# Optimization experiments

Hardware: AMD Instinct MI355X
Metric: run time of the kernel (lower is better)

## Reference

```python
import jax, jax.numpy as jnp
import numpy as np

B, CIN, X, Y = 4, 3, 128, 128
D, L, DEPTH, OUT = 64, 8, 4, 1
GRID_RANGE = 1.0
LN_EPS = 1e-5
YR = Y // 2 + 1


def _build_phi_f():
    # 1D Hilbert-matrix eigenbases along each axis, outer product, then rfft2.
    def top_eigvecs(n):
        i = np.arange(n)
        Z = 1.0 / (i[:, None] + i[None, :] + 1.0)  # Hilbert matrix, float64
        w, V = np.linalg.eigh(Z)
        idx = np.argsort(-w)[:L]
        return V.T[idx]  # (L, n)

    Vx = top_eigvecs(X)
    Vy = top_eigvecs(Y)
    phi = Vx[:, :, None] * Vy[:, None, :]  # (L, X, Y) separable eigenfunctions
    Phi_f = np.fft.rfft2(phi, s=(X, Y))  # (L, X, YR)
    return jnp.asarray(Phi_f, dtype=jnp.complex64)


def setup_inputs() -> dict:
    key = jax.random.key(0)
    ks = jax.random.split(key, 16)
    u = lambda k, shape, bound: jax.random.uniform(k, shape, jnp.float32, -bound, bound)
    inv = 1.0 / np.sqrt(D)
    inp = {
        "x": jax.random.normal(ks[0], (B, CIN, X, Y), jnp.float32),
        "Phi_f": _build_phi_f(),  # constant buffer
        "lift_w": u(ks[1], (D, CIN + 2), 1.0 / np.sqrt(CIN + 2)),
        "lift_b": u(ks[2], (D,), 1.0 / np.sqrt(CIN + 2)),
        "Theta": u(ks[3], (DEPTH, L, D, D), 1.0 / D),  # kaiming_uniform(a=sqrt(5)) ~ U(-1/d, 1/d)
        "glu_val_w": u(ks[4], (DEPTH, D, D), inv),
        "glu_val_b": u(ks[5], (DEPTH, D), inv),
        "glu_gate_w": u(ks[6], (DEPTH, D, D), inv),
        "glu_gate_b": u(ks[7], (DEPTH, D), inv),
        "ln_g": jnp.ones((DEPTH, D), jnp.float32),
        "ln_b": jnp.zeros((DEPTH, D), jnp.float32),
        "head_w": u(ks[8], (OUT, D), inv),
        "head_b": u(ks[9], (OUT,), inv),
    }
    return inp


def _stu_layer(h, Phi_f, Theta, vw, vb, gw, gb, g, b):
    # LayerNorm over channel dim (torch LayerNorm on channels-last view)
    ht = jnp.transpose(h, (0, 2, 3, 1))  # (B, X, Y, D)
    mu = jnp.mean(ht, axis=-1, keepdims=True)
    var = jnp.var(ht, axis=-1, keepdims=True)
    zt = (ht - mu) * jax.lax.rsqrt(var + LN_EPS) * g + b
    z = jnp.transpose(zt, (0, 3, 1, 2))  # (B, D, X, Y)

    Xf = jnp.fft.rfftn(z, axes=(-2, -1))  # (B, D, X, YR) complex
    Uf = Xf[:, :, None, :, :] * jnp.conj(Phi_f)[None, None]  # (B, D, L, X, YR)
    U = jnp.fft.irfftn(Uf, s=(X, Y), axes=(-2, -1))  # (B, D, L, X, Y)
    # einsum('bdlxy,lhd->bhlxy') followed by sum over l, fused:
    S = jnp.einsum("bdlxy,lhd->bhxy", U, Theta)

    V = jnp.einsum("bhxy,oh->boxy", S, vw) + vb[None, :, None, None]
    G = jax.nn.sigmoid(jnp.einsum("bhxy,oh->boxy", S, gw) + gb[None, :, None, None])
    return h + V * G


def reference(x, Phi_f, lift_w, lift_b, Theta, glu_val_w, glu_val_b,
              glu_gate_w, glu_gate_b, ln_g, ln_b, head_w, head_b):
    bsz = x.shape[0]
    # add_2d_grid: append yy, xx coordinate channels
    ys = jnp.linspace(0.0, GRID_RANGE, X, dtype=x.dtype)
    xs = jnp.linspace(0.0, GRID_RANGE, Y, dtype=x.dtype)
    yy, xx = jnp.meshgrid(ys, xs, indexing="ij")
    yy = jnp.broadcast_to(yy[None, None], (bsz, 1, X, Y))
    xx = jnp.broadcast_to(xx[None, None], (bsz, 1, X, Y))
    h = jnp.concatenate([x, yy, xx], axis=1)  # (B, CIN+2, X, Y)

    # LocalLift2D with kernel_size=1 -> pointwise conv
    h = jnp.einsum("bcxy,dc->bdxy", h, lift_w) + lift_b[None, :, None, None]

    for i in range(DEPTH):
        h = _stu_layer(h, Phi_f, Theta[i], glu_val_w[i], glu_val_b[i],
                       glu_gate_w[i], glu_gate_b[i], ln_g[i], ln_b[i])

    y = jnp.einsum("bdxy,od->boxy", h, head_w) + head_b[None, :, None, None]
    return y
```

## Files before the change

### kernel.cpp

```cpp
#include <hip/hip_runtime.h>
#include <math.h>
#include <string.h>


#define NXY 16384

#define OFF_V       16
#define OFF_MC      1040
#define OFF_THETAA  132112
#define OFF_AG      263184
#define OFF_Z       295952
#define OFF_S       2393104
#define OFF_H       4490256
#define OFF_P       8684560
#define WS_NEED_F   25461776ULL

typedef short short8 __attribute__((ext_vector_type(8)));
typedef float float4m __attribute__((ext_vector_type(4)));

__device__ __forceinline__ unsigned short bf_rn(float f) {
    unsigned u = __float_as_uint(f);
    u += 0x7fffu + ((u >> 16) & 1u);
    return (unsigned short)(u >> 16);
}
__device__ __forceinline__ float bf_tof(unsigned short s) {
    return __uint_as_float(((unsigned)s) << 16);
}

__global__ void poison_out(float* out) { out[0] = 1e9f; }


static float vhost[1024];
static float* d_v_dev = nullptr;

static void host_hilbert_topk(float* outv) {
    static double Vs[8][128];
    static double W[8][128];
    double recip[256];
    for (int i = 0; i < 256; i++) recip[i] = 1.0 / (double)(i + 1);
    for (int j = 0; j < 8; j++)
        for (int i = 0; i < 128; i++) Vs[j][i] = recip[i + j];
    for (int outer = 0; outer < 25; outer++) {
        for (int half = 0; half < 2; half++) {
            for (int j = 0; j < 8; j++)
                for (int i = 0; i < 128; i++) {
                    double s = 0.0;
                    for (int k = 0; k < 128; k++) s += Vs[j][k] * recip[i + k];
                    W[j][i] = s;
                }
            memcpy(Vs, W, sizeof(Vs));
        }
        for (int j = 0; j < 8; j++) {
            for (int p = 0; p < j; p++) {
                double d = 0.0;
                for (int i = 0; i < 128; i++) d += Vs[j][i] * Vs[p][i];
                for (int i = 0; i < 128; i++) Vs[j][i] -= d * Vs[p][i];
            }
            double nn = 0.0;
            for (int i = 0; i < 128; i++) nn += Vs[j][i] * Vs[j][i];
            double inv = 1.0 / sqrt(nn);
            for (int i = 0; i < 128; i++) Vs[j][i] *= inv;
        }
    }
    for (int j = 0; j < 8; j++)
        for (int i = 0; i < 128; i++) outv[j * 128 + i] = (float)Vs[j][i];
}

namespace {
struct VInit {
    VInit() {
        host_hilbert_topk(vhost);
        float* p = nullptr;
        if (hipMalloc((void**)&p, sizeof(vhost)) == hipSuccess && p != nullptr) {
            if (hipMemcpy(p, vhost, sizeof(vhost), hipMemcpyHostToDevice) == hipSuccess) {
                d_v_dev = p;
            } else {
                (void)hipFree(p);
                d_v_dev = nullptr;
            }
        }
    }
};
VInit vinit_once;
}

__global__ void build_mct(const float* __restrict__ v, unsigned short* __restrict__ McT) {
    int l = blockIdx.y;
    int idx = blockIdx.x * 256 + threadIdx.x;
    int r = idx >> 7, k = idx & 127;
    McT[l * 16384 + idx] = bf_rn(v[l * 128 + ((k - r) & 127)]);
}


__global__ void build_thetaAHL(const float* __restrict__ Theta, unsigned short* __restrict__ ThA) {
    int i = blockIdx.x * 256 + threadIdx.x;
    int k = i & 127; int r = i >> 7;
    int m = r & 127; r >>= 7;
    int tile = r & 3; int dep = r >> 2;
    int l2 = m >> 6, hch = m & 63, d = k & 63;
    float f = Theta[(((dep * 8 + tile * 2 + l2) * 64) + hch) * 64 + d];
    unsigned short hb = bf_rn(f);
    ThA[i] = (k < 64) ? hb : bf_rn(f - bf_tof(hb));
}

__global__ void build_AG(const float* __restrict__ vw, const float* __restrict__ gw,
                         float* __restrict__ AG) {
    int i = blockIdx.x * 256 + threadIdx.x;
    int m = i & 127; int r = i >> 7; int h = r & 63; int dep = r >> 6;
    int o = m >> 1;
    const float* W = (m & 1) ? gw : vw;
    AG[i] = W[(dep * 64 + o) * 64 + h];
}


__global__ void lift_ln(const float* __restrict__ x, const float* __restrict__ lw,
                        const float* __restrict__ lb, const float* __restrict__ g0,
                        const float* __restrict__ b0, float* __restrict__ h,
                        unsigned short* __restrict__ zT) {
    __shared__ float w[320];
    __shared__ float bsm[64];
    __shared__ float gs[64], bs[64];
    int tid = threadIdx.x;
    for (int i = tid; i < 320; i += 256) w[i] = lw[i];
    if (tid < 64) { bsm[tid] = lb[tid]; gs[tid] = g0[tid]; bs[tid] = b0[tid]; }
    __syncthreads();
    int b = blockIdx.y;
    int xy = blockIdx.x * 256 + tid;
    int xi = xy >> 7, yi = xy & 127;
    float c0 = x[(size_t)(b * 3 + 0) * NXY + xy];
    float c1 = x[(size_t)(b * 3 + 1) * NXY + xy];
    float c2 = x[(size_t)(b * 3 + 2) * NXY + xy];
    float yyv = xi * (1.0f / 127.0f), xxv = yi * (1.0f / 127.0f);
    float vv[64];
    float sum = 0.f;
#pragma unroll
    for (int d = 0; d < 64; d++) {
        float acc = bsm[d] + w[d * 5] * c0 + w[d * 5 + 1] * c1 + w[d * 5 + 2] * c2
                  + w[d * 5 + 3] * yyv + w[d * 5 + 4] * xxv;
        vv[d] = acc;
        sum += acc;
        h[(size_t)(b * 64 + d) * NXY + xy] = acc;
    }
    float mu = sum * (1.0f / 64.0f);
    float vs = 0.f;
#pragma unroll
    for (int d = 0; d < 64; d++) { float t = vv[d] - mu; vs += t * t; }
    float inv = rsqrtf(vs * (1.0f / 64.0f) + 1e-5f);
    unsigned short t16[64];
#pragma unroll
    for (int d = 0; d < 64; d++) t16[d] = bf_rn((vv[d] - mu) * inv * gs[d] + bs[d]);
    unsigned short* zp = zT + ((size_t)b * NXY + xy) * 64;
#pragma unroll
    for (int i = 0; i < 8; i++) {
        uint4 pk;
        pk.x = (unsigned)t16[8 * i + 0] | ((unsigned)t16[8 * i + 1] << 16);
        pk.y = (unsigned)t16[8 * i + 2] | ((unsigned)t16[8 * i + 3] << 16);
        pk.z = (unsigned)t16[8 * i + 4] | ((unsigned)t16[8 * i + 5] << 16);
        pk.w = (unsigned)t16[8 * i + 6] | ((unsigned)t16[8 * i + 7] << 16);
        *(uint4*)(zp + 8 * i) = pk;
    }
}

__device__ __forceinline__ int sw_idx(int row, int k) {
    return row * 128 + ((((k >> 3) ^ (row & 7)) << 3) | (k & 7));
}
__device__ __forceinline__ int sw64(int row, int k) {
    return row * 64 + (((((k >> 3) ^ (row & 7)) & 7) << 3) | (k & 7));
}


__launch_bounds__(256)
__global__ void k1_mfma(const unsigned short* __restrict__ zT,
                        const unsigned short* __restrict__ ThA,
                        unsigned short* __restrict__ P) {
    __shared__ unsigned short st[16384];
    const int lhtile = blockIdx.x, x = blockIdx.y, b = blockIdx.z;
    const int tid = threadIdx.x;
    const int wid = tid >> 6, lane = tid & 63;
    const int ln15 = lane & 15, q = lane >> 4;
    const int ko = q * 8;
    const unsigned short* Ab = ThA + lhtile * 16384;
    const unsigned short* Bb = zT + ((size_t)b * NXY + x * 128) * 64;

    float4m acc[2][8];
#pragma unroll
    for (int mt = 0; mt < 2; mt++)
#pragma unroll
        for (int nt = 0; nt < 8; nt++) acc[mt][nt] = (float4m){0.f, 0.f, 0.f, 0.f};

#pragma unroll
    for (int k0 = 0; k0 < 128; k0 += 32) {
        short8 a[2];
#pragma unroll
        for (int mt = 0; mt < 2; mt++)
            a[mt] = *(const short8*)(Ab + (wid * 32 + mt * 16 + ln15) * 128 + k0 + ko);
        int d0 = (k0 & 63) + ko;
#pragma unroll
        for (int nt = 0; nt < 8; nt++) {
            int n = nt * 16 + ln15;
            short8 bf = *(const short8*)(Bb + n * 64 + d0);
#pragma unroll
            for (int mt = 0; mt < 2; mt++)
                acc[mt][nt] = __builtin_amdgcn_mfma_f32_16x16x32_bf16(a[mt], bf, acc[mt][nt], 0, 0, 0);
        }
    }
#pragma unroll
    for (int mt = 0; mt < 2; mt++)
#pragma unroll
        for (int nt = 0; nt < 8; nt++) {
            int y = nt * 16 + ln15;
            int r0 = wid * 32 + mt * 16 + q * 4;
            float av[4] = {acc[mt][nt].x, acc[mt][nt].y, acc[mt][nt].z, acc[mt][nt].w};
#pragma unroll
            for (int r = 0; r < 4; r++) st[sw_idx(r0 + r, y)] = bf_rn(av[r]);
        }
    __syncthreads();
    unsigned short* Pb = P + (size_t)(b * 512 + lhtile * 128) * NXY + x * 128;
#pragma unroll
    for (int i = 0; i < 8; i++) {
        int idx = i * 256 + tid;
        int m = idx >> 4, c = idx & 15;
        *(uint4*)(Pb + (size_t)m * NXY + c * 8) = *(const uint4*)&st[sw_idx(m, c * 8)];
    }
}


__launch_bounds__(256)
__global__ void corrsum_ys(const unsigned short* __restrict__ P,
                           const unsigned short* __restrict__ McT,
                           unsigned short* __restrict__ S) {
    __shared__ unsigned short Tt[8192];
    const int hh = blockIdx.x, yh = blockIdx.y, b = blockIdx.z;
    const int tid = threadIdx.x;
    const int wid = tid >> 6, lane = tid & 63;
    const int ln15 = lane & 15, q = lane >> 4;
    const int ko = q * 8;
    const int mrow0 = wid * 32 + ln15;
    const int yb = yh * 64;

    float4m accS[2][4];
#pragma unroll
    for (int mt = 0; mt < 2; mt++)
#pragma unroll
        for (int nt = 0; nt < 4; nt++) accS[mt][nt] = (float4m){0.f, 0.f, 0.f, 0.f};

    short8 apre[2][4][2];

    {
        const unsigned short* pl = P + ((size_t)(b * 8 + 0) * 64 + hh) * NXY;
#pragma unroll
        for (int k4 = 0; k4 < 4; k4++)
#pragma unroll
            for (int mt = 0; mt < 2; mt++)
                apre[0][k4][mt] = *(const short8*)(pl + (mrow0 + mt * 16) * 128 + k4 * 32 + ko);
    }

#pragma unroll
    for (int l = 0; l < 8; l++) {
        const unsigned short* Mc = McT + l * 16384;
        const int cb = l & 1, nb = cb ^ 1;

        float4m acc1[2][4];
#pragma unroll
        for (int mt = 0; mt < 2; mt++)
#pragma unroll
            for (int nt = 0; nt < 4; nt++) acc1[mt][nt] = (float4m){0.f, 0.f, 0.f, 0.f};
#pragma unroll
        for (int k4 = 0; k4 < 4; k4++) {
            int k0 = k4 * 32;
#pragma unroll
            for (int nt = 0; nt < 4; nt++) {
                int n = yb + nt * 16 + ln15;
                short8 bf = *(const short8*)(Mc + n * 128 + k0 + ko);
#pragma unroll
                for (int mt = 0; mt < 2; mt++)
                    acc1[mt][nt] = __builtin_amdgcn_mfma_f32_16x16x32_bf16(apre[cb][k4][mt], bf, acc1[mt][nt], 0, 0, 0);
            }
        }
#pragma unroll
        for (int mt = 0; mt < 2; mt++)
#pragma unroll
            for (int nt = 0; nt < 4; nt++) {
                int yo = nt * 16 + ln15;
                int x0 = wid * 32 + mt * 16 + q * 4;
                float av[4] = {acc1[mt][nt].x, acc1[mt][nt].y, acc1[mt][nt].z, acc1[mt][nt].w};
                unsigned short hs[4];
#pragma unroll
                for (int r = 0; r < 4; r++) hs[r] = bf_rn(av[r]);
                uint2 pk;
                pk.x = (unsigned)hs[0] | ((unsigned)hs[1] << 16);
                pk.y = (unsigned)hs[2] | ((unsigned)hs[3] << 16);
                *(uint2*)&Tt[sw_idx(yo, x0)] = pk;
            }
        __syncthreads();

        if (l < 7) {
            const unsigned short* pln = P + ((size_t)(b * 8 + l + 1) * 64 + hh) * NXY;
#pragma unroll
            for (int k4 = 0; k4 < 4; k4++)
#pragma unroll
                for (int mt = 0; mt < 2; mt++)
                    apre[nb][k4][mt] = *(const short8*)(pln + (mrow0 + mt * 16) * 128 + k4 * 32 + ko);
        }

#pragma unroll
        for (int k4 = 0; k4 < 4; k4++) {
            int k0 = k4 * 32;
            short8 a2[2];
#pragma unroll
            for (int mt = 0; mt < 2; mt++)
                a2[mt] = *(const short8*)(Mc + (mrow0 + mt * 16) * 128 + k0 + ko);
#pragma unroll
            for (int nt = 0; nt < 4; nt++) {
                int n = nt * 16 + ln15;
                short8 bf = *(const short8*)&Tt[sw_idx(n, k0 + ko)];
#pragma unroll
                for (int mt = 0; mt < 2; mt++)
                    accS[mt][nt] = __builtin_amdgcn_mfma_f32_16x16x32_bf16(a2[mt], bf, accS[mt][nt], 0, 0, 0);
            }
        }
        __syncthreads();
    }

#pragma unroll
    for (int mt = 0; mt < 2; mt++)
#pragma unroll
        for (int nt = 0; nt < 4; nt++) {
            int yl = nt * 16 + ln15;
            int x0 = wid * 32 + mt * 16 + q * 4;
            float av[4] = {accS[mt][nt].x, accS[mt][nt].y, accS[mt][nt].z, accS[mt][nt].w};
#pragma unroll
            for (int r = 0; r < 4; r++) Tt[sw64(x0 + r, yl)] = bf_rn(av[r]);
        }
    __syncthreads();
    unsigned short* Sb = S + ((size_t)(b * 64) + hh) * NXY + yb;
#pragma unroll
    for (int i = 0; i < 4; i++) {
        int idx = i * 256 + tid;
        int xr = idx >> 3, c = idx & 7;
        *(uint4*)(Sb + xr * 128 + c * 8) = *(const uint4*)&Tt[sw64(xr, c * 8)];
    }
}


template <int KTOT, long long BS1, long long PSTR, int NPART>
__launch_bounds__(256)
__global__ void glu_ln(const float* __restrict__ A0,
                       const unsigned short* __restrict__ B0, long long bsx, long long bsz,
                       float* __restrict__ C0, long long csx, long long csz, long long csm,
                       const float* __restrict__ e_vb, const float* __restrict__ e_gb,
                       const float* __restrict__ lngn, const float* __restrict__ lnbn,
                       unsigned short* __restrict__ zT,
                       const float* __restrict__ hw, const float* __restrict__ hbp,
                       float* __restrict__ outp) {
    constexpr int KS = 16;
    __shared__ float As[KS][132];
    __shared__ float Bs[KS][132];
    __shared__ float hn[64][129];
    const int tid = threadIdx.x;
    const int tm = tid >> 4, tn = tid & 15;
    const int m0 = tm * 8, n0 = tn * 8;
    const float* Ab = A0;
    const unsigned short* Bb = B0 + (long long)blockIdx.x * bsx + (long long)blockIdx.z * bsz;
    float* Cb = C0 + (long long)blockIdx.x * csx + (long long)blockIdx.z * csz;

    float acc[8][8];
#pragma unroll
    for (int i = 0; i < 8; i++)
#pragma unroll
        for (int j = 0; j < 8; j++) acc[i][j] = 0.f;

    for (int k0 = 0; k0 < KTOT; k0 += KS) {
#pragma unroll
        for (int i = 0; i < 2; i++) {
            int idx = tid + i * 256;
            int k = idx >> 5, f4 = (idx & 31) * 4;
            float4 v = *(const float4*)(Ab + (long long)(k0 + k) * 128 + f4);
            *(float4*)&As[k][f4] = v;
        }
#pragma unroll
        for (int i = 0; i < 2; i++) {
            int idx = tid + i * 256;
            int k = idx >> 5, f4 = (idx & 31) * 4;
            const unsigned short* bp = Bb + (long long)(k0 + k) * BS1 + f4;
            float vx = 0.f, vy = 0.f, vz = 0.f, vw = 0.f;
#pragma unroll
            for (int p = 0; p < NPART; p++) {
                uint2 t = *(const uint2*)(bp + (long long)p * PSTR);
                vx += bf_tof((unsigned short)(t.x & 0xffff));
                vy += bf_tof((unsigned short)(t.x >> 16));
                vz += bf_tof((unsigned short)(t.y & 0xffff));
                vw += bf_tof((unsigned short)(t.y >> 16));
            }
            Bs[k][f4] = vx; Bs[k][f4 + 1] = vy; Bs[k][f4 + 2] = vz; Bs[k][f4 + 3] = vw;
        }
        __syncthreads();
#pragma unroll
        for (int kk = 0; kk < KS; kk++) {
            float4 a0 = *(const float4*)&As[kk][m0];
            float4 a1 = *(const float4*)&As[kk][m0 + 4];
            float4 b0 = *(const float4*)&Bs[kk][n0];
            float4 b1 = *(const float4*)&Bs[kk][n0 + 4];
            float av[8] = {a0.x, a0.y, a0.z, a0.w, a1.x, a1.y, a1.z, a1.w};
            float bv[8] = {b0.x, b0.y, b0.z, b0.w, b1.x, b1.y, b1.z, b1.w};
#pragma unroll
            for (int i = 0; i < 8; i++)
#pragma unroll
                for (int j = 0; j < 8; j++) acc[i][j] += av[i] * bv[j];
        }
        __syncthreads();
    }

#pragma unroll
    for (int i = 0; i < 4; i++) {
        int o = (m0 >> 1) + i;
        float vbv = e_vb[o], gbv = e_gb[o];
        float* hp = Cb + (long long)o * csm + n0;
        float4 h0 = *(float4*)hp;
        float4 h1 = *(float4*)(hp + 4);
        float hv[8] = {h0.x, h0.y, h0.z, h0.w, h1.x, h1.y, h1.z, h1.w};
#pragma unroll
        for (int j = 0; j < 8; j++) {
            float V = acc[2 * i][j] + vbv;
            float G = acc[2 * i + 1][j] + gbv;
            float s = 1.0f / (1.0f + expf(-G));
            hv[j] += V * s;
            hn[o][n0 + j] = hv[j];
        }
        if (outp == nullptr) {
            float4 o0 = {hv[0], hv[1], hv[2], hv[3]};
            float4 o1 = {hv[4], hv[5], hv[6], hv[7]};
            *(float4*)hp = o0;
            *(float4*)(hp + 4) = o1;
        }
    }

    if (lngn != nullptr) {
        __syncthreads();
        if (tid < 128) {
            int xy = tid;
            float sum = 0.f;
#pragma unroll
            for (int d = 0; d < 64; d++) sum += hn[d][xy];
            float mu = sum * (1.0f / 64.0f);
            float vs = 0.f;
#pragma unroll
            for (int d = 0; d < 64; d++) { float t = hn[d][xy] - mu; vs += t * t; }
            float inv = rsqrtf(vs * (1.0f / 64.0f) + 1e-5f);
            unsigned short t16[64];
#pragma unroll
            for (int d = 0; d < 64; d++)
                t16[d] = bf_rn((hn[d][xy] - mu) * inv * lngn[d] + lnbn[d]);
            unsigned short* zp = zT + ((size_t)blockIdx.z * NXY + blockIdx.x * 128 + xy) * 64;
#pragma unroll
            for (int i = 0; i < 8; i++) {
                uint4 pk;
                pk.x = (unsigned)t16[8 * i + 0] | ((unsigned)t16[8 * i + 1] << 16);
                pk.y = (unsigned)t16[8 * i + 2] | ((unsigned)t16[8 * i + 3] << 16);
                pk.z = (unsigned)t16[8 * i + 4] | ((unsigned)t16[8 * i + 5] << 16);
                pk.w = (unsigned)t16[8 * i + 6] | ((unsigned)t16[8 * i + 7] << 16);
                *(uint4*)(zp + 8 * i) = pk;
            }
        }
    } else if (outp != nullptr) {
        __syncthreads();
        if (tid < 128) {
            int xy = tid;
            float acch = hbp[0];
#pragma unroll
            for (int d = 0; d < 64; d++) acch += hn[d][xy] * hw[d];
            outp[(size_t)blockIdx.z * NXY + blockIdx.x * 128 + xy] = acch;
        }
    }
}


extern "C" void kernel_launch(void* const* d_in, const int* in_sizes, int n_in,
                              void* d_out, int out_size, void* d_ws, size_t ws_size,
                              hipStream_t stream) {
    const float* x      = (const float*)d_in[0];
    const float* lift_w = (const float*)d_in[2];
    const float* lift_b = (const float*)d_in[3];
    const float* Theta  = (const float*)d_in[4];
    const float* vw     = (const float*)d_in[5];
    const float* vb     = (const float*)d_in[6];
    const float* gw     = (const float*)d_in[7];
    const float* gb     = (const float*)d_in[8];
    const float* ln_g   = (const float*)d_in[9];
    const float* ln_b   = (const float*)d_in[10];
    const float* head_w = (const float*)d_in[11];
    const float* head_b = (const float*)d_in[12];
    float* out = (float*)d_out;
    float* ws = (float*)d_ws;
    (void)in_sizes; (void)n_in; (void)out_size;

    unsigned short* McT = (unsigned short*)(ws + OFF_MC);
    unsigned short* ThA = (unsigned short*)(ws + OFF_THETAA);
    float* AG     = ws + OFF_AG;
    unsigned short* zT = (unsigned short*)(ws + OFF_Z);
    unsigned short* S  = (unsigned short*)(ws + OFF_S);
    float* h      = ws + OFF_H;
    unsigned short* P = (unsigned short*)(ws + OFF_P);

    const float* vdev = d_v_dev;
    if (vdev == nullptr) {
        float* v = ws + OFF_V;
        hipMemcpyAsync(v, vhost, sizeof(vhost), hipMemcpyHostToDevice, stream);
        vdev = v;
    }

    build_mct<<<dim3(64, 8), 256, 0, stream>>>(vdev, McT);
    build_thetaAHL<<<1024, 256, 0, stream>>>(Theta, ThA);
    build_AG<<<128, 256, 0, stream>>>(vw, gw, AG);

    lift_ln<<<dim3(64, 4), 256, 0, stream>>>(x, lift_w, lift_b, ln_g, ln_b, h, zT);

    for (int dep = 0; dep < 4; dep++) {
        k1_mfma<<<dim3(4, 128, 4), 256, 0, stream>>>(zT, ThA + dep * 65536, P);

        corrsum_ys<<<dim3(64, 2, 4), 256, 0, stream>>>(P, McT, S);

        const float* lngn = (dep < 3) ? (ln_g + (dep + 1) * 64) : nullptr;
        const float* lnbn = (dep < 3) ? (ln_b + (dep + 1) * 64) : nullptr;
        float* outp = (dep == 3) ? out : nullptr;
        glu_ln<64, 16384LL, 0LL, 1><<<dim3(128, 1, 4), 256, 0, stream>>>(
            AG + dep * 8192,
            S, 128, 1048576,
            h, 128, 1048576, 16384,
            vb + dep * 64, gb + dep * 64,
            lngn, lnbn, zT,
            head_w, head_b, outp);
    }

    if (ws_size < WS_NEED_F * 4ULL) {
        poison_out<<<1, 1, 0, stream>>>(out);
    }
}
```

Baseline: 553.8 us.

## Split correlation second GEMM over K per wave to remove per-iteration barriers

The second-stage GEMM in the correlation kernel is restructured so each wave contracts only over its own 32 x-rows (its K slice) into a full 128x64 partial accumulator. This removes the two __syncthreads per l-iteration, since each wave only reads the Tt region it wrote itself. A shared-memory reduction across the four waves is added at the end. The trade-off is a much larger accumulator footprint per wave (32 float4 tiles), which raises register pressure, plus 32KB of extra LDS and a serial 3-step merge. The software prefetch of the next P plane is also dropped.

```diff
diff --git a/kernel.cpp b/kernel.cpp
--- a/kernel.cpp
+++ b/kernel.cpp
@@ -226,39 +226,36 @@
 
 
 __launch_bounds__(256)
-__global__ void corrsum_ys(const unsigned short* __restrict__ P,
-                           const unsigned short* __restrict__ McT,
-                           unsigned short* __restrict__ S) {
+__global__ void corr_nb(const unsigned short* __restrict__ P,
+                        const unsigned short* __restrict__ McT,
+                        unsigned short* __restrict__ S) {
     __shared__ unsigned short Tt[8192];
+    __shared__ float Mrg[8192];
     const int hh = blockIdx.x, yh = blockIdx.y, b = blockIdx.z;
     const int tid = threadIdx.x;
     const int wid = tid >> 6, lane = tid & 63;
     const int ln15 = lane & 15, q = lane >> 4;
     const int ko = q * 8;
-    const int mrow0 = wid * 32 + ln15;
+    const int xq0 = wid * 32;
     const int yb = yh * 64;
 
-    float4m accS[2][4];
-#pragma unroll
-    for (int mt = 0; mt < 2; mt++)
-#pragma unroll
-        for (int nt = 0; nt < 4; nt++) accS[mt][nt] = (float4m){0.f, 0.f, 0.f, 0.f};
-
-    short8 apre[2][4][2];
-
-    {
-        const unsigned short* pl = P + ((size_t)(b * 8 + 0) * 64 + hh) * NXY;
-#pragma unroll
-        for (int k4 = 0; k4 < 4; k4++)
-#pragma unroll
-            for (int mt = 0; mt < 2; mt++)
-                apre[0][k4][mt] = *(const short8*)(pl + (mrow0 + mt * 16) * 128 + k4 * 32 + ko);
-    }
+    float4m acc[8][4];
+#pragma unroll
+    for (int mtu = 0; mtu < 8; mtu++)
+#pragma unroll
+        for (int nt = 0; nt < 4; nt++) acc[mtu][nt] = (float4m){0.f, 0.f, 0.f, 0.f};
 
 #pragma unroll
     for (int l = 0; l < 8; l++) {
         const unsigned short* Mc = McT + l * 16384;
-        const int cb = l & 1, nb = cb ^ 1;
+        const unsigned short* pl = P + ((size_t)(b * 8 + l) * 64 + hh) * NXY;
+
+        short8 ap[4][2];
+#pragma unroll
+        for (int k4 = 0; k4 < 4; k4++)
+#pragma unroll
+            for (int mt = 0; mt < 2; mt++)
+                ap[k4][mt] = *(const short8*)(pl + (xq0 + mt * 16 + ln15) * 128 + k4 * 32 + ko);
 
         float4m acc1[2][4];
 #pragma unroll
@@ -274,7 +271,7 @@
                 short8 bf = *(const short8*)(Mc + n * 128 + k0 + ko);
 #pragma unroll
                 for (int mt = 0; mt < 2; mt++)
-                    acc1[mt][nt] = __builtin_amdgcn_mfma_f32_16x16x32_bf16(apre[cb][k4][mt], bf, acc1[mt][nt], 0, 0, 0);
+                    acc1[mt][nt] = __builtin_amdgcn_mfma_f32_16x16x32_bf16(ap[k4][mt], bf, acc1[mt][nt], 0, 0, 0);
             }
         }
 #pragma unroll
@@ -282,7 +279,7 @@
 #pragma unroll
             for (int nt = 0; nt < 4; nt++) {
                 int yo = nt * 16 + ln15;
-                int x0 = wid * 32 + mt * 16 + q * 4;
+                int x0 = xq0 + mt * 16 + q * 4;
                 float av[4] = {acc1[mt][nt].x, acc1[mt][nt].y, acc1[mt][nt].z, acc1[mt][nt].w};
                 unsigned short hs[4];
 #pragma unroll
@@ -292,46 +289,63 @@
                 pk.y = (unsigned)hs[2] | ((unsigned)hs[3] << 16);
                 *(uint2*)&Tt[sw_idx(yo, x0)] = pk;
             }
+
+        short8 a2[8];
+#pragma unroll
+        for (int mtu = 0; mtu < 8; mtu++)
+            a2[mtu] = *(const short8*)(Mc + (mtu * 16 + ln15) * 128 + xq0 + ko);
+#pragma unroll
+        for (int nt = 0; nt < 4; nt++) {
+            short8 bf = *(const short8*)&Tt[sw_idx(nt * 16 + ln15, xq0 + ko)];
+#pragma unroll
+            for (int mtu = 0; mtu < 8; mtu++)
+                acc[mtu][nt] = __builtin_amdgcn_mfma_f32_16x16x32_bf16(a2[mtu], bf, acc[mtu][nt], 0, 0, 0);
+        }
+    }
+
+    __syncthreads();
+#pragma unroll
+    for (int src = 1; src < 4; src++) {
+        if (wid == src) {
+#pragma unroll
+            for (int mtu = 0; mtu < 8; mtu++)
+#pragma unroll
+                for (int nt = 0; nt < 4; nt++) {
+                    int v0 = (mtu * 4 + nt) * 4;
+                    Mrg[(v0 + 0) * 64 + lane] = acc[mtu][nt].x;
+                    Mrg[(v0 + 1) * 64 + lane] = acc[mtu][nt].y;
+                    Mrg[(v0 + 2) * 64 + lane] = acc[mtu][nt].z;
+                    Mrg[(v0 + 3) * 64 + lane] = acc[mtu][nt].w;
+                }
+        }
         __syncthreads();
-
-        if (l < 7) {
-            const unsigned short* pln = P + ((size_t)(b * 8 + l + 1) * 64 + hh) * NXY;
-#pragma unroll
-            for (int k4 = 0; k4 < 4; k4++)
-#pragma unroll
-                for (int mt = 0; mt < 2; mt++)
-                    apre[nb][k4][mt] = *(const short8*)(pln + (mrow0 + mt * 16) * 128 + k4 * 32 + ko);
-        }
-
-#pragma unroll
-        for (int k4 = 0; k4 < 4; k4++) {
-            int k0 = k4 * 32;
-            short8 a2[2];
-#pragma unroll
-            for (int mt = 0; mt < 2; mt++)
-                a2[mt] = *(const short8*)(Mc + (mrow0 + mt * 16) * 128 + k0 + ko);
+        if (wid == 0) {
+#pragma unroll
+            for (int mtu = 0; mtu < 8; mtu++)
+#pragma unroll
+                for (int nt = 0; nt < 4; nt++) {
+                    int v0 = (mtu * 4 + nt) * 4;
+                    acc[mtu][nt].x += Mrg[(v0 + 0) * 64 + lane];
+                    acc[mtu][nt].y += Mrg[(v0 + 1) * 64 + lane];
+                    acc[mtu][nt].z += Mrg[(v0 + 2) * 64 + lane];
+                    acc[mtu][nt].w += Mrg[(v0 + 3) * 64 + lane];
+                }
+        }
+        __syncthreads();
+    }
+
+    if (wid == 0) {
+#pragma unroll
+        for (int mtu = 0; mtu < 8; mtu++)
 #pragma unroll
             for (int nt = 0; nt < 4; nt++) {
-                int n = nt * 16 + ln15;
-                short8 bf = *(const short8*)&Tt[sw_idx(n, k0 + ko)];
-#pragma unroll
-                for (int mt = 0; mt < 2; mt++)
-                    accS[mt][nt] = __builtin_amdgcn_mfma_f32_16x16x32_bf16(a2[mt], bf, accS[mt][nt], 0, 0, 0);
-            }
-        }
-        __syncthreads();
-    }
-
-#pragma unroll
-    for (int mt = 0; mt < 2; mt++)
-#pragma unroll
-        for (int nt = 0; nt < 4; nt++) {
-            int yl = nt * 16 + ln15;
-            int x0 = wid * 32 + mt * 16 + q * 4;
-            float av[4] = {accS[mt][nt].x, accS[mt][nt].y, accS[mt][nt].z, accS[mt][nt].w};
-#pragma unroll
-            for (int r = 0; r < 4; r++) Tt[sw64(x0 + r, yl)] = bf_rn(av[r]);
-        }
+                int yl = nt * 16 + ln15;
+                int u0 = mtu * 16 + q * 4;
+                float av[4] = {acc[mtu][nt].x, acc[mtu][nt].y, acc[mtu][nt].z, acc[mtu][nt].w};
+#pragma unroll
+                for (int r = 0; r < 4; r++) Tt[sw64(u0 + r, yl)] = bf_rn(av[r]);
+            }
+    }
     __syncthreads();
     unsigned short* Sb = S + ((size_t)(b * 64) + hh) * NXY + yb;
 #pragma unroll
@@ -518,7 +532,7 @@
     for (int dep = 0; dep < 4; dep++) {
         k1_mfma<<<dim3(4, 128, 4), 256, 0, stream>>>(zT, ThA + dep * 65536, P);
 
-        corrsum_ys<<<dim3(64, 2, 4), 256, 0, stream>>>(P, McT, S);
+        corr_nb<<<dim3(64, 2, 4), 256, 0, stream>>>(P, McT, S);
 
         const float* lngn = (dep < 3) ? (ln_g + (dep + 1) * 64) : nullptr;
         const float* lnbn = (dep < 3) ? (ln_b + (dep + 1) * 64) : nullptr;
```

New measurement: 599.8 us. +8.3%, slower.
